# Performance work log

Measured on AMD Instinct MI355X. Metric: run time of the kernel, lower is better.

The kernel has to match this reference:

```python
import jax, jax.numpy as jnp
import numpy as np

D_MODEL = 2048
NUM_HEADS = 16
HEAD_DIM = D_MODEL // NUM_HEADS  # 128


def setup_inputs() -> dict:
    key = jax.random.key(0)
    ks = jax.random.split(key, 11)
    B, S = 2, 2048
    s = 0.02
    return {
        "q": jax.random.normal(ks[0], (B, S, D_MODEL), jnp.float32),
        "k": jax.random.normal(ks[1], (B, S, D_MODEL), jnp.float32),
        "v": jax.random.normal(ks[2], (B, S, D_MODEL), jnp.float32),
        "Wq": jax.random.normal(ks[3], (D_MODEL, D_MODEL), jnp.float32) * s,
        "bq": jnp.zeros((D_MODEL,), jnp.float32),
        "Wk": jax.random.normal(ks[4], (D_MODEL, HEAD_DIM), jnp.float32) * s,
        "bk": jnp.zeros((HEAD_DIM,), jnp.float32),
        "Wv": jax.random.normal(ks[5], (D_MODEL, HEAD_DIM), jnp.float32) * s,
        "bv": jnp.zeros((HEAD_DIM,), jnp.float32),
        "Wo": jax.random.normal(ks[6], (D_MODEL, D_MODEL), jnp.float32) * s,
        "bo": jnp.zeros((D_MODEL,), jnp.float32),
    }


def reference(q, k, v, Wq, bq, Wk, bk, Wv, bv, Wo, bo):
    B, Sq, _ = q.shape
    Skv = k.shape[1]
    # Query projection -> per-head queries [B, H, Sq, Dh]
    qh = (q @ Wq + bq).reshape(B, Sq, NUM_HEADS, HEAD_DIM).transpose(0, 2, 1, 3)
    # Shared single-head K/V projections [B, Skv, Dh]
    kh = k @ Wk + bk
    vh = v @ Wv + bv
    scale = 1.0 / jnp.sqrt(jnp.asarray(HEAD_DIM, qh.dtype))
    # MQA: broadcast shared K over heads without materializing per-head copies
    scores = jnp.einsum("bhqd,bkd->bhqk", qh, kh) * scale  # [B, H, Sq, Skv]
    attn = jax.nn.softmax(scores, axis=-1)
    out = jnp.einsum("bhqk,bkd->bhqd", attn, vh)  # [B, H, Sq, Dh]
    out = out.transpose(0, 2, 1, 3).reshape(B, Sq, D_MODEL)
    return out @ Wo + bo
```

## Files before the change

### kernel.cpp

```cpp
#include <hip/hip_runtime.h>

typedef unsigned short u16;
typedef unsigned int u32;
typedef __bf16 bf16_t;
typedef __attribute__((ext_vector_type(8))) bf16_t bf16x8;
typedef __attribute__((ext_vector_type(4))) float f32x4;

__device__ inline u16 f2bf(float f) {
    union { float f; u32 u; } v; v.f = f;
    u32 u = v.u;
    u32 r = (u + 0x7fffu + ((u >> 16) & 1u)) >> 16;
    return (u16)r;
}

__device__ inline void async_cp16(const void* g, void* l) {
    __builtin_amdgcn_global_load_lds((const __attribute__((address_space(1))) void*)g,
                                     (__attribute__((address_space(3))) void*)l, 16, 0, 0);
}

__global__ __launch_bounds__(256) void cvt3(const float* __restrict__ a,
                                            const float* __restrict__ b,
                                            const float* __restrict__ c,
                                            u16* __restrict__ oa, u16* __restrict__ ob,
                                            u16* __restrict__ oc) {
    int z = blockIdx.y;
    const float* in = z == 0 ? a : (z == 1 ? b : c);
    u16* out = z == 0 ? oa : (z == 1 ? ob : oc);
    int i = (blockIdx.x * 256 + threadIdx.x) * 4;
    float4 f = *(const float4*)(in + i);
    ushort4 o;
    o.x = f2bf(f.x); o.y = f2bf(f.y); o.z = f2bf(f.z); o.w = f2bf(f.w);
    *(ushort4*)(out + i) = o;
}

__global__ __launch_bounds__(256) void transpose2(const float* __restrict__ W0,
                                                  u16* __restrict__ T0,
                                                  const float* __restrict__ W1,
                                                  u16* __restrict__ T1,
                                                  int K, int N) {
    const float* W = blockIdx.z == 0 ? W0 : W1;
    u16* WT = blockIdx.z == 0 ? T0 : T1;
    __shared__ float tile[32][33];
    int tr0 = blockIdx.x * 32;
    int tc0 = blockIdx.y * 32;
    int t = threadIdx.x;
    for (int i = 0; i < 4; i++) {
        int idx = t + i * 256; int r = idx >> 5, c = idx & 31;
        tile[r][c] = W[(size_t)(tr0 + r) * N + tc0 + c];
    }
    __syncthreads();
    for (int i = 0; i < 4; i++) {
        int idx = t + i * 256; int r = idx >> 5, c = idx & 31;
        WT[(size_t)(tc0 + r) * K + tr0 + c] = f2bf(tile[c][r]);
    }
}

template <typename OUT_T>
__global__ __launch_bounds__(512, 2) void gemm_bt2(const u16* __restrict__ A,
                                                   const u16* __restrict__ BT,
                                                   const float* __restrict__ bias,
                                                   OUT_T* __restrict__ C,
                                                   int M, int N, int K, int ldout) {
    __shared__ u16 smem[3 * 24576];
    int t = threadIdx.x, lane = t & 63, wv = t >> 6;
    int quad = lane >> 4, c16 = lane & 15;
    int rx = c16 & 7;
    int wr = wv >> 1, wc = wv & 1;

    int nwg = gridDim.x;
    int cpx = nwg >> 3;
    int bid = blockIdx.x;
    int swz = (bid & 7) * cpx + (bid >> 3);
    int Mt = M >> 8;
    int bm = (swz % Mt) << 8;
    int bn = (swz / Mt) << 7;

    f32x4 acc[4][4] = {};

    int srow = wv * 8 + (lane >> 3);
    int scol = ((lane & 7) ^ (lane >> 3)) * 8;
    const u16* Ag = A + (size_t)(bm + srow) * K + scol;
    const u16* Bg = BT + (size_t)(bn + srow) * K + scol;

    auto STAGE = [&](int kt, int d) {
        u16* base = smem + d * 24576;
        u16* ad = base + (size_t)(wv * 8) * 64;
        u16* bd = base + 16384 + (size_t)(wv * 8) * 64;
        const u16* ag = Ag + (size_t)kt * 64;
        const u16* bg = Bg + (size_t)kt * 64;
        for (int p = 0; p < 4; p++)
            async_cp16(ag + (size_t)(p * 64) * K, ad + p * 4096);
        for (int p = 0; p < 2; p++)
            async_cp16(bg + (size_t)(p * 64) * K, bd + p * 4096);
    };

    const int NT = K >> 6;
    STAGE(0, 0);
    STAGE(1, 1);

    for (int tt = 0; tt < NT; tt++) {
        if (tt + 1 < NT) asm volatile("s_waitcnt vmcnt(6)" ::: "memory");
        else             asm volatile("s_waitcnt vmcnt(0)" ::: "memory");
        __builtin_amdgcn_s_barrier();
        if (tt + 2 < NT) STAGE(tt + 2, (tt + 2) % 3);

        const u16* sA = smem + (tt % 3) * 24576;
        const u16* sB = sA + 16384;

        for (int rh = 0; rh < 2; rh++) {
            bf16x8 af[2][2];
            for (int mi = 0; mi < 2; mi++)
                for (int kk = 0; kk < 2; kk++)
                    af[mi][kk] = *(const bf16x8*)&sA[(wr * 64 + rh * 32 + mi * 16 + c16) * 64 +
                                                     (((kk * 4 + quad) ^ rx) * 8)];
            for (int ch = 0; ch < 2; ch++) {
                bf16x8 bf[2][2];
                for (int ni = 0; ni < 2; ni++)
                    for (int kk = 0; kk < 2; kk++)
                        bf[ni][kk] = *(const bf16x8*)&sB[(wc * 64 + ch * 32 + ni * 16 + c16) * 64 +
                                                         (((kk * 4 + quad) ^ rx) * 8)];
                __builtin_amdgcn_s_setprio(1);
                for (int kk = 0; kk < 2; kk++)
                    for (int mi = 0; mi < 2; mi++)
                        for (int ni = 0; ni < 2; ni++)
                            acc[rh * 2 + mi][ch * 2 + ni] = __builtin_amdgcn_mfma_f32_16x16x32_bf16(
                                af[mi][kk], bf[ni][kk], acc[rh * 2 + mi][ch * 2 + ni], 0, 0, 0);
                __builtin_amdgcn_s_setprio(0);
            }
        }
    }

    for (int mi = 0; mi < 4; mi++) {
        for (int ni = 0; ni < 4; ni++) {
            int col = bn + wc * 64 + ni * 16 + c16;
            float bv = bias[col];
            for (int p = 0; p < 4; p++) {
                int row = bm + wr * 64 + mi * 16 + quad * 4 + p;
                float v = acc[mi][ni][p] + bv;
                size_t off = (size_t)row * ldout + col;
                if constexpr (__is_same(OUT_T, u16)) C[off] = f2bf(v);
                else C[off] = v;
            }
        }
    }
}

__global__ __launch_bounds__(256) void gemm_kv_sk(const u16* __restrict__ kbf,
                                                  const u16* __restrict__ vbf,
                                                  const u16* __restrict__ WkT,
                                                  const u16* __restrict__ WvT,
                                                  float* __restrict__ kacc,
                                                  float* __restrict__ vacc,
                                                  int K, int KS) {
    bool isv = blockIdx.y == 1;
    const u16* A = isv ? vbf : kbf;
    const u16* BT = isv ? WvT : WkT;
    float* aco = isv ? vacc : kacc;
    __shared__ u16 sA[128 * 32];
    __shared__ u16 sB[128 * 32];
    int t = threadIdx.x, lane = t & 63, wv = t >> 6;
    int quad = lane >> 4, c16 = lane & 15;
    int bm = blockIdx.x * 128;
    int wm = (wv & 1) * 64, wn = (wv >> 1) * 64;
    f32x4 acc[4][4] = {};

    int srow = wv * 32 + (lane >> 2);
    int scol = (lane & 3) * 8;
    const u16* Ag = A + (size_t)(bm + srow) * K + scol;
    const u16* Bg = BT + (size_t)srow * K + scol;
    u16* sAd = &sA[(wv * 32) * 32];
    u16* sBd = &sB[(wv * 32) * 32];

    int kbeg = blockIdx.z * KS;
    for (int k0 = kbeg; k0 < kbeg + KS; k0 += 32) {
        __syncthreads();
        async_cp16(Ag + k0, sAd);
        async_cp16(Ag + (size_t)16 * K + k0, sAd + 16 * 32);
        async_cp16(Bg + k0, sBd);
        async_cp16(Bg + (size_t)16 * K + k0, sBd + 16 * 32);
        __syncthreads();
        bf16x8 af[4], bfr[4];
        for (int mi = 0; mi < 4; mi++)
            af[mi] = *(const bf16x8*)&sA[(wm + mi * 16 + c16) * 32 + quad * 8];
        for (int ni = 0; ni < 4; ni++)
            bfr[ni] = *(const bf16x8*)&sB[(wn + ni * 16 + c16) * 32 + quad * 8];
        for (int mi = 0; mi < 4; mi++)
            for (int ni = 0; ni < 4; ni++)
                acc[mi][ni] = __builtin_amdgcn_mfma_f32_16x16x32_bf16(
                    af[mi], bfr[ni], acc[mi][ni], 0, 0, 0);
    }

    for (int mi = 0; mi < 4; mi++)
        for (int ni = 0; ni < 4; ni++) {
            int col = wn + ni * 16 + c16;
            for (int p = 0; p < 4; p++) {
                int row = bm + wm + mi * 16 + quad * 4 + p;
                atomicAdd(&aco[(size_t)row * 128 + col], acc[mi][ni][p]);
            }
        }
}

__global__ __launch_bounds__(256) void cvt_kv(const float* __restrict__ kacc,
                                              const float* __restrict__ vacc,
                                              const float* __restrict__ bk,
                                              const float* __restrict__ bv,
                                              u16* __restrict__ khb,
                                              u16* __restrict__ vhT,
                                              int M) {
    int t = threadIdx.x;
    int tr0 = blockIdx.x * 32;
    int tc0 = blockIdx.y * 32;
    if (blockIdx.z == 0) {
        for (int i = 0; i < 4; i++) {
            int idx = t + i * 256; int r = idx >> 5, c = idx & 31;
            khb[(size_t)(tr0 + r) * 128 + tc0 + c] =
                f2bf(kacc[(size_t)(tr0 + r) * 128 + tc0 + c] + bk[tc0 + c]);
        }
    } else {
        __shared__ float tile[32][33];
        for (int i = 0; i < 4; i++) {
            int idx = t + i * 256; int r = idx >> 5, c = idx & 31;
            tile[r][c] = vacc[(size_t)(tr0 + r) * 128 + tc0 + c] + bv[tc0 + c];
        }
        __syncthreads();
        for (int i = 0; i < 4; i++) {
            int idx = t + i * 256; int r = idx >> 5, c = idx & 31;
            vhT[(size_t)(tc0 + r) * M + tr0 + c] = f2bf(tile[c][r]);
        }
    }
}

__global__ __launch_bounds__(256, 2) void mqa_attn(const u16* __restrict__ qh,
                                                   const u16* __restrict__ kh,
                                                   const u16* __restrict__ vhT,
                                                   u16* __restrict__ outp,
                                                   int S) {
    constexpr float CEXP = 0.08838834764831845f * 1.4426950408889634f;
    __shared__ u16 smem[40960];
    u16* sK0 = smem;
    u16* sV0 = smem + 16384;
    u16* sP  = smem + 32768;

    int t = threadIdx.x, lane = t & 63, wv = t >> 6;
    int quad = lane >> 4, c16 = lane & 15;
    int rx = c16 & 7;
    int b = blockIdx.z, h = blockIdx.y;
    int q0w = blockIdx.x * 128 + wv * 32;
    int BS = b * S;

    bf16x8 aq[2][4];
    for (int mi = 0; mi < 2; mi++) {
        const u16* qp = qh + (size_t)(BS + q0w + mi * 16 + c16) * 2048 + h * 128 + quad * 8;
        for (int c = 0; c < 4; c++) aq[mi][c] = *(const bf16x8*)(qp + c * 32);
    }

    f32x4 out[2][8] = {};
    f32x4 lsumv[2] = {};
    u16* sPw = sP + wv * 2048;

    int ksub = lane >> 4, kch = lane & 15;
    int klx = (wv * 4 + ksub) & 7;
    const u16* kgb = kh + (size_t)(BS + wv * 4 + ksub) * 128 + ((kch ^ klx) * 8);
    int vsub = lane >> 3, vch = lane & 7;
    int vlx = vsub & 7;
    const u16* vgb = vhT + (size_t)(wv * 8 + vsub) * 4096 + BS + ((vch ^ vlx) * 8);

    u16* kb0 = sK0 + (wv * 4) * 128;
    u16* vb0 = sV0 + (wv * 8) * 64;

    auto STAGE = [&](int kv0, int d) {
        u16* kb = kb0 + d * 8192;
        u16* vb = vb0 + d * 8192;
        for (int p = 0; p < 4; p++)
            async_cp16(kgb + (size_t)(kv0 + p * 16) * 128, kb + p * 2048);
        for (int p = 0; p < 4; p++)
            async_cp16(vgb + (size_t)(p * 32) * 4096 + kv0, vb + p * 2048);
    };

    const int NT = S >> 6;
    STAGE(0, 0);
    __syncthreads();

    for (int tt = 0; tt < NT; tt++) {
        int cur = tt & 1;
        if (tt + 1 < NT) STAGE((tt + 1) * 64, cur ^ 1);
        const u16* sKc = sK0 + cur * 8192;
        const u16* sVc = sV0 + cur * 8192;

        for (int ni = 0; ni < 4; ni++) {
            f32x4 sc[2] = {};
            const u16* kr = sKc + (ni * 16 + c16) * 128;
            for (int c = 0; c < 4; c++) {
                bf16x8 bk = *(const bf16x8*)(kr + ((c * 4 + quad) ^ rx) * 8);
                sc[0] = __builtin_amdgcn_mfma_f32_16x16x32_bf16(bk, aq[0][c], sc[0], 0, 0, 0);
                sc[1] = __builtin_amdgcn_mfma_f32_16x16x32_bf16(bk, aq[1][c], sc[1], 0, 0, 0);
            }
            for (int mi = 0; mi < 2; mi++) {
                u32 eu[4];
                f32x4 et;
                for (int p = 0; p < 4; p++) {
                    float e = __builtin_amdgcn_exp2f(sc[mi][p] * CEXP);
                    union { float f; u32 u; } cv; cv.f = e;
                    eu[p] = cv.u;
                    cv.u &= 0xffff0000u;
                    et[p] = cv.f;
                }
                lsumv[mi] += et;
                u32 pk0 = __builtin_amdgcn_perm(eu[1], eu[0], 0x07060302u);
                u32 pk1 = __builtin_amdgcn_perm(eu[3], eu[2], 0x07060302u);
                *(uint2*)&sPw[(mi * 16 + c16) * 64 +
                              (((ni * 2 + (quad >> 1)) ^ rx) * 8) + (quad & 1) * 4] =
                    make_uint2(pk0, pk1);
            }
        }
        asm volatile("s_waitcnt lgkmcnt(0)" ::: "memory");

        for (int ks = 0; ks < 2; ks++) {
            int kchu = ((ks * 4 + quad) ^ rx) * 8;
            bf16x8 ap0 = *(const bf16x8*)&sPw[(0 * 16 + c16) * 64 + kchu];
            bf16x8 ap1 = *(const bf16x8*)&sPw[(1 * 16 + c16) * 64 + kchu];
            for (int ni = 0; ni < 8; ni++) {
                bf16x8 bv = *(const bf16x8*)(sVc + (ni * 16 + c16) * 64 + kchu);
                out[0][ni] = __builtin_amdgcn_mfma_f32_16x16x32_bf16(ap0, bv, out[0][ni], 0, 0, 0);
                out[1][ni] = __builtin_amdgcn_mfma_f32_16x16x32_bf16(ap1, bv, out[1][ni], 0, 0, 0);
            }
        }

        __syncthreads();
    }

    float lp[2];
    for (int mi = 0; mi < 2; mi++) {
        float x = lsumv[mi][0] + lsumv[mi][1] + lsumv[mi][2] + lsumv[mi][3];
        x += __shfl_xor(x, 16, 64);
        x += __shfl_xor(x, 32, 64);
        lp[mi] = x;
    }
    for (int mi = 0; mi < 2; mi++) {
        float inv[4];
        for (int p = 0; p < 4; p++)
            inv[p] = 1.f / __shfl(lp[mi], quad * 4 + p, 64);
        u16* op = outp + (size_t)(BS + q0w + mi * 16 + quad * 4) * 2048 + h * 128;
        for (int ni = 0; ni < 8; ni++)
            for (int p = 0; p < 4; p++)
                op[(size_t)p * 2048 + ni * 16 + c16] = f2bf(out[mi][ni][p] * inv[p]);
    }
}

extern "C" void kernel_launch(void* const* d_in, const int* in_sizes, int n_in,
                              void* d_out, int out_size, void* d_ws, size_t ws_size,
                              hipStream_t stream) {
    const float* q  = (const float*)d_in[0];
    const float* k  = (const float*)d_in[1];
    const float* v  = (const float*)d_in[2];
    const float* Wq = (const float*)d_in[3];
    const float* bq = (const float*)d_in[4];
    const float* Wk = (const float*)d_in[5];
    const float* bk = (const float*)d_in[6];
    const float* Wv = (const float*)d_in[7];
    const float* bv = (const float*)d_in[8];
    const float* Wo = (const float*)d_in[9];
    const float* bo = (const float*)d_in[10];
    float* out = (float*)d_out;

    const int S = 2048, D = 2048, Dh = 128, M = 4096;
    const int QKV = M * D;
    const int WDD = D * D;
    const int WDH = D * Dh;
    const int MDh = M * Dh;

    u16* ws   = (u16*)d_ws;
    u16* q_bf = ws;
    u16* k_bf = q_bf + QKV;
    u16* v_bf = k_bf + QKV;
    u16* WqT  = v_bf + QKV;
    u16* WoT  = WqT + WDD;
    u16* WkT  = WoT + WDD;
    u16* WvT  = WkT + WDH;
    u16* qhb  = WvT + WDH;
    u16* khb  = qhb + QKV;
    u16* vhTb = khb + MDh;
    u16* aout = vhTb + MDh;
    float* kacc = (float*)(aout + QKV);
    float* vacc = kacc + MDh;

    hipMemsetAsync(kacc, 0, (size_t)2 * MDh * sizeof(float), stream);

    cvt3<<<dim3(QKV / 1024, 3), 256, 0, stream>>>(q, k, v, q_bf, k_bf, v_bf);
    transpose2<<<dim3(64, 64, 2), 256, 0, stream>>>(Wq, WqT, Wo, WoT, D, D);
    transpose2<<<dim3(64, 4, 2), 256, 0, stream>>>(Wk, WkT, Wv, WvT, D, Dh);

    gemm_bt2<u16><<<dim3(256), 512, 0, stream>>>(q_bf, WqT, bq, qhb, M, D, D, D);
    gemm_kv_sk<<<dim3(32, 2, 4), 256, 0, stream>>>(k_bf, v_bf, WkT, WvT, kacc, vacc, D, 512);
    cvt_kv<<<dim3(128, 4, 2), 256, 0, stream>>>(kacc, vacc, bk, bv, khb, vhTb, M);

    mqa_attn<<<dim3(16, 16, 2), 256, 0, stream>>>(qhb, khb, vhTb, aout, S);

    gemm_bt2<float><<<dim3(256), 512, 0, stream>>>(aout, WoT, bo, out, M, D, D, D);
}
```

Baseline: 366.2 us.

## Use 32x32 MFMA with in-register P via permlane32 swap in MQA attention

Result: no change. 361.3 us (-1.3%).

```diff
diff --git a/kernel.cpp b/kernel.cpp
--- a/kernel.cpp
+++ b/kernel.cpp
@@ -5,12 +5,20 @@
 typedef __bf16 bf16_t;
 typedef __attribute__((ext_vector_type(8))) bf16_t bf16x8;
 typedef __attribute__((ext_vector_type(4))) float f32x4;
+typedef __attribute__((ext_vector_type(16))) float f32x16;
+typedef __attribute__((ext_vector_type(2))) unsigned int u32x2;
 
 __device__ inline u16 f2bf(float f) {
     union { float f; u32 u; } v; v.f = f;
     u32 u = v.u;
     u32 r = (u + 0x7fffu + ((u >> 16) & 1u)) >> 16;
     return (u16)r;
+}
+
+__device__ inline u32 cvt_pk_bf16(float lo, float hi) {
+    u32 r;
+    asm("v_cvt_pk_bf16_f32 %0, %1, %2" : "=v"(r) : "v"(lo), "v"(hi));
+    return r;
 }
 
 __device__ inline void async_cp16(const void* g, void* l) {
@@ -67,13 +75,11 @@
     int rx = c16 & 7;
     int wr = wv >> 1, wc = wv & 1;
 
-    int nwg = gridDim.x;
-    int cpx = nwg >> 3;
     int bid = blockIdx.x;
-    int swz = (bid & 7) * cpx + (bid >> 3);
-    int Mt = M >> 8;
-    int bm = (swz % Mt) << 8;
-    int bn = (swz / Mt) << 7;
+    int xcd = bid & 7;
+    int loc = bid >> 3;
+    int bm = (((xcd >> 1) << 2) + (loc & 3)) << 8;
+    int bn = (((xcd & 1) << 3) + (loc >> 2)) << 7;
 
     f32x4 acc[4][4] = {};
 
@@ -236,27 +242,26 @@
                                                    u16* __restrict__ outp,
                                                    int S) {
     constexpr float CEXP = 0.08838834764831845f * 1.4426950408889634f;
-    __shared__ u16 smem[40960];
+    __shared__ u16 smem[32768];
     u16* sK0 = smem;
     u16* sV0 = smem + 16384;
-    u16* sP  = smem + 32768;
 
     int t = threadIdx.x, lane = t & 63, wv = t >> 6;
-    int quad = lane >> 4, c16 = lane & 15;
-    int rx = c16 & 7;
-    int b = blockIdx.z, h = blockIdx.y;
+    int l31 = lane & 31, hh = lane >> 5;
+    int lx = l31 & 7;
+    int b = blockIdx.z, hb = blockIdx.y;
     int q0w = blockIdx.x * 128 + wv * 32;
     int BS = b * S;
 
-    bf16x8 aq[2][4];
-    for (int mi = 0; mi < 2; mi++) {
-        const u16* qp = qh + (size_t)(BS + q0w + mi * 16 + c16) * 2048 + h * 128 + quad * 8;
-        for (int c = 0; c < 4; c++) aq[mi][c] = *(const bf16x8*)(qp + c * 32);
-    }
-
-    f32x4 out[2][8] = {};
-    f32x4 lsumv[2] = {};
-    u16* sPw = sP + wv * 2048;
+    bf16x8 aq[8];
+    {
+        const u16* qp = qh + (size_t)(BS + q0w + l31) * 2048 + hb * 128 + hh * 8;
+#pragma unroll
+        for (int st = 0; st < 8; st++) aq[st] = *(const bf16x8*)(qp + st * 16);
+    }
+
+    f32x16 accO[4] = {};
+    float lsum = 0.f;
 
     int ksub = lane >> 4, kch = lane & 15;
     int klx = (wv * 4 + ksub) & 7;
@@ -287,63 +292,73 @@
         const u16* sKc = sK0 + cur * 8192;
         const u16* sVc = sV0 + cur * 8192;
 
-        for (int ni = 0; ni < 4; ni++) {
-            f32x4 sc[2] = {};
-            const u16* kr = sKc + (ni * 16 + c16) * 128;
-            for (int c = 0; c < 4; c++) {
-                bf16x8 bk = *(const bf16x8*)(kr + ((c * 4 + quad) ^ rx) * 8);
-                sc[0] = __builtin_amdgcn_mfma_f32_16x16x32_bf16(bk, aq[0][c], sc[0], 0, 0, 0);
-                sc[1] = __builtin_amdgcn_mfma_f32_16x16x32_bf16(bk, aq[1][c], sc[1], 0, 0, 0);
-            }
-            for (int mi = 0; mi < 2; mi++) {
-                u32 eu[4];
-                f32x4 et;
-                for (int p = 0; p < 4; p++) {
-                    float e = __builtin_amdgcn_exp2f(sc[mi][p] * CEXP);
-                    union { float f; u32 u; } cv; cv.f = e;
-                    eu[p] = cv.u;
-                    cv.u &= 0xffff0000u;
-                    et[p] = cv.f;
-                }
-                lsumv[mi] += et;
-                u32 pk0 = __builtin_amdgcn_perm(eu[1], eu[0], 0x07060302u);
-                u32 pk1 = __builtin_amdgcn_perm(eu[3], eu[2], 0x07060302u);
-                *(uint2*)&sPw[(mi * 16 + c16) * 64 +
-                              (((ni * 2 + (quad >> 1)) ^ rx) * 8) + (quad & 1) * 4] =
-                    make_uint2(pk0, pk1);
-            }
-        }
-        asm volatile("s_waitcnt lgkmcnt(0)" ::: "memory");
-
-        for (int ks = 0; ks < 2; ks++) {
-            int kchu = ((ks * 4 + quad) ^ rx) * 8;
-            bf16x8 ap0 = *(const bf16x8*)&sPw[(0 * 16 + c16) * 64 + kchu];
-            bf16x8 ap1 = *(const bf16x8*)&sPw[(1 * 16 + c16) * 64 + kchu];
-            for (int ni = 0; ni < 8; ni++) {
-                bf16x8 bv = *(const bf16x8*)(sVc + (ni * 16 + c16) * 64 + kchu);
-                out[0][ni] = __builtin_amdgcn_mfma_f32_16x16x32_bf16(ap0, bv, out[0][ni], 0, 0, 0);
-                out[1][ni] = __builtin_amdgcn_mfma_f32_16x16x32_bf16(ap1, bv, out[1][ni], 0, 0, 0);
+        bf16x8 pf[4];
+#pragma unroll
+        for (int sub = 0; sub < 2; sub++) {
+            f32x16 accS = {};
+            const u16* krow = sKc + (size_t)(sub * 32 + l31) * 128;
+#pragma unroll
+            for (int st = 0; st < 8; st++) {
+                bf16x8 kf = *(const bf16x8*)(krow + (((st * 2 + hh) ^ lx) * 8));
+                accS = __builtin_amdgcn_mfma_f32_32x32x16_bf16(kf, aq[st], accS, 0, 0, 0);
+            }
+            u32 P[8];
+#pragma unroll
+            for (int g = 0; g < 4; g++) {
+                float e0 = __builtin_amdgcn_exp2f(accS[4 * g + 0] * CEXP);
+                float e1 = __builtin_amdgcn_exp2f(accS[4 * g + 1] * CEXP);
+                float e2 = __builtin_amdgcn_exp2f(accS[4 * g + 2] * CEXP);
+                float e3 = __builtin_amdgcn_exp2f(accS[4 * g + 3] * CEXP);
+                P[2 * g] = cvt_pk_bf16(e0, e1);
+                P[2 * g + 1] = cvt_pk_bf16(e2, e3);
+            }
+#pragma unroll
+            for (int w = 0; w < 8; w++) {
+                union { u32 u; float f; } lo, hi;
+                lo.u = P[w] << 16;
+                hi.u = P[w] & 0xffff0000u;
+                lsum += lo.f + hi.f;
+            }
+            u32x2 a0 = __builtin_amdgcn_permlane32_swap(P[0], P[2], false, false);
+            u32x2 a1 = __builtin_amdgcn_permlane32_swap(P[1], P[3], false, false);
+            u32x2 a2 = __builtin_amdgcn_permlane32_swap(P[4], P[6], false, false);
+            u32x2 a3 = __builtin_amdgcn_permlane32_swap(P[5], P[7], false, false);
+            union { u32 u[4]; bf16x8 v; } f0, f1;
+            f0.u[0] = a0.x; f0.u[1] = a1.x; f0.u[2] = a0.y; f0.u[3] = a1.y;
+            f1.u[0] = a2.x; f1.u[1] = a3.x; f1.u[2] = a2.y; f1.u[3] = a3.y;
+            pf[sub * 2] = f0.v;
+            pf[sub * 2 + 1] = f1.v;
+        }
+
+#pragma unroll
+        for (int db = 0; db < 4; db++) {
+            const u16* vrow = sVc + (size_t)(db * 32 + l31) * 64;
+#pragma unroll
+            for (int ks = 0; ks < 4; ks++) {
+                bf16x8 vf = *(const bf16x8*)(vrow + (((ks * 2 + hh) ^ lx) * 8));
+                accO[db] = __builtin_amdgcn_mfma_f32_32x32x16_bf16(pf[ks], vf, accO[db], 0, 0, 0);
             }
         }
 
         __syncthreads();
     }
 
-    float lp[2];
-    for (int mi = 0; mi < 2; mi++) {
-        float x = lsumv[mi][0] + lsumv[mi][1] + lsumv[mi][2] + lsumv[mi][3];
-        x += __shfl_xor(x, 16, 64);
-        x += __shfl_xor(x, 32, 64);
-        lp[mi] = x;
-    }
-    for (int mi = 0; mi < 2; mi++) {
-        float inv[4];
-        for (int p = 0; p < 4; p++)
-            inv[p] = 1.f / __shfl(lp[mi], quad * 4 + p, 64);
-        u16* op = outp + (size_t)(BS + q0w + mi * 16 + quad * 4) * 2048 + h * 128;
-        for (int ni = 0; ni < 8; ni++)
-            for (int p = 0; p < 4; p++)
-                op[(size_t)p * 2048 + ni * 16 + c16] = f2bf(out[mi][ni][p] * inv[p]);
+    lsum += __shfl_xor(lsum, 32, 64);
+    float invq = 1.f / lsum;
+    float inv[16];
+#pragma unroll
+    for (int r = 0; r < 16; r++) {
+        int qloc = (r & 3) + 8 * (r >> 2) + 4 * hh;
+        inv[r] = __shfl(invq, qloc, 64);
+    }
+#pragma unroll
+    for (int db = 0; db < 4; db++) {
+#pragma unroll
+        for (int r = 0; r < 16; r++) {
+            int qloc = (r & 3) + 8 * (r >> 2) + 4 * hh;
+            outp[(size_t)(BS + q0w + qloc) * 2048 + hb * 128 + db * 32 + l31] =
+                f2bf(accO[db][r] * inv[r]);
+        }
     }
 }
 
```
